# Optimization experiments

Measured on AMD Instinct MI355X. Metric: run time of the kernel, lower is better.

The kernel has to match this reference:

```python
import jax, jax.numpy as jnp
from jax import lax
import numpy as np

B, T, F, H = 1024, 512, 64, 128


def setup_inputs() -> dict:
    key = jax.random.key(0)
    ks = jax.random.split(key, 12)
    s_in = 1.0 / np.sqrt(H)  # PyTorch LSTM init scale
    inp = {
        "x": jax.random.normal(ks[0], (B, T, F), dtype=jnp.float32),
        # layer 0 (gate order i, f, g, o as in PyTorch)
        "W_ih0": jax.random.uniform(ks[1], (4 * H, F), jnp.float32, -s_in, s_in),
        "W_hh0": jax.random.uniform(ks[2], (4 * H, H), jnp.float32, -s_in, s_in),
        "b_ih0": jax.random.uniform(ks[3], (4 * H,), jnp.float32, -s_in, s_in),
        "b_hh0": jax.random.uniform(ks[4], (4 * H,), jnp.float32, -s_in, s_in),
        # layer 1
        "W_ih1": jax.random.uniform(ks[5], (4 * H, H), jnp.float32, -s_in, s_in),
        "W_hh1": jax.random.uniform(ks[6], (4 * H, H), jnp.float32, -s_in, s_in),
        "b_ih1": jax.random.uniform(ks[7], (4 * H,), jnp.float32, -s_in, s_in),
        "b_hh1": jax.random.uniform(ks[8], (4 * H,), jnp.float32, -s_in, s_in),
        # MLP head
        "fc1_w": jax.random.uniform(ks[9], (64, H), jnp.float32, -s_in, s_in),
        "fc1_b": jnp.zeros((64,), jnp.float32),
        "fc2_w": jax.random.uniform(ks[10], (1, 64), jnp.float32, -1 / 8.0, 1 / 8.0),
        "fc2_b": jnp.zeros((1,), jnp.float32),
    }
    return inp


def _lstm_layer(x_seq, W_ih, W_hh, b_ih, b_hh):
    """x_seq: [B, T, Fin] -> hidden sequence [B, T, H]. PyTorch gate order i,f,g,o."""
    Bn = x_seq.shape[0]
    Hn = W_hh.shape[1]
    # precompute input projection for all timesteps (one big GEMM)
    x_proj = jnp.einsum("btf,gf->btg", x_seq, W_ih) + b_ih + b_hh  # [B, T, 4H]

    def step(carry, xt):
        h, c = carry
        gates = xt + h @ W_hh.T  # [B, 4H]
        i, f, g, o = jnp.split(gates, 4, axis=-1)
        i = jax.nn.sigmoid(i)
        f = jax.nn.sigmoid(f)
        g = jnp.tanh(g)
        o = jax.nn.sigmoid(o)
        c = f * c + i * g
        h = o * jnp.tanh(c)
        return (h, c), h

    h0 = jnp.zeros((Bn, Hn), x_seq.dtype)
    c0 = jnp.zeros((Bn, Hn), x_seq.dtype)
    (_, _), hs = lax.scan(step, (h0, c0), jnp.swapaxes(x_proj, 0, 1))  # hs: [T, B, H]
    return jnp.swapaxes(hs, 0, 1)


def reference(x, W_ih0, W_hh0, b_ih0, b_hh0, W_ih1, W_hh1, b_ih1, b_hh1,
              fc1_w, fc1_b, fc2_w, fc2_b):
    h1 = _lstm_layer(x, W_ih0, W_hh0, b_ih0, b_hh0)   # [B, T, H]
    h2 = _lstm_layer(h1, W_ih1, W_hh1, b_ih1, b_hh1)  # [B, T, H]
    last = h2[:, -1, :]                                # [B, H]
    out = jax.nn.relu(last @ fc1_w.T + fc1_b)          # [B, 64]
    out = out @ fc2_w.T + fc2_b                        # [B, 1]
    return out
```

## Files before the change

kernel.cpp:

```cpp
#include <hip/hip_runtime.h>
#include <math.h>


#define BB 1024
#define TT 512
#define FF 64
#define HH 128
#define LOG2E 1.44269504088896340736f
#define TWOLOG2E 2.88539008177792681472f

typedef __attribute__((ext_vector_type(8))) short     v8s;
typedef __attribute__((ext_vector_type(8))) _Float16  v8h;
typedef __attribute__((ext_vector_type(4))) float     v4f;

__device__ __forceinline__ short bf16r(float v) {
    unsigned u = __float_as_uint(v);
    return (short)((u + 0x7FFFu + ((u >> 16) & 1u)) >> 16);
}
__device__ __forceinline__ float bf16tof(short s) {
    return __uint_as_float(((unsigned)(unsigned short)s) << 16);
}
__device__ __forceinline__ float rcp1p(float y) {
    return __builtin_amdgcn_rcpf(1.0f + __builtin_exp2f(y));
}
__device__ __forceinline__ void light_barrier() {
    asm volatile("s_waitcnt lgkmcnt(0)\n\ts_barrier" ::: "memory");
}
__device__ __forceinline__ void wait_flag_ge(int* f, int need) {
    for (int i = 0; i < 2000000; ++i) {
        int v = __hip_atomic_fetch_add(f, 0, __ATOMIC_ACQUIRE,
                                       __HIP_MEMORY_SCOPE_AGENT);
        if (v >= need) return;
        __builtin_amdgcn_s_sleep(4);
    }
}
__device__ __forceinline__ void split2(float a, float b,
                                       unsigned& hi, unsigned& lo) {
    unsigned ua = __float_as_uint(a), ub = __float_as_uint(b);
    hi = (ua >> 16) | (ub & 0xFFFF0000u);
    float ra = a - __uint_as_float(ua & 0xFFFF0000u);
    float rb = b - __uint_as_float(ub & 0xFFFF0000u);
    lo = (__float_as_uint(ra) >> 16) | (__float_as_uint(rb) & 0xFFFF0000u);
}


#define PROD_STEP(CUR, NXT, RD, WR, tv, PUB)                                   \
  {                                                                            \
    float2 xnew = *(const float2*)xp;                                          \
    if ((tv) < TT - 4) xp += FF;                                               \
    if ((tv) > 0) {                                                            \
      uint2 hv = *(const uint2*)&hbuf[CUR][hrow * 136 + hcol];                 \
      *(uint2*)hcs = hv;                                                       \
      hcs += (long)BB * HH;                                                    \
    }                                                                          \
    v8h ah[4];                                                                 \
    _Pragma("unroll") for (int q = 0; q < 4; ++q)                              \
        ah[q] = *(const v8h*)&hbuf[CUR][lane16 * 136 + q * 32 + quad * 8];     \
    v4f g0 = xacc[0], g1 = xacc[1], g2 = xacc[2], g3 = xacc[3];                \
    _Pragma("unroll") for (int q = 0; q < 4; ++q) {                            \
      g0 = __builtin_amdgcn_mfma_f32_16x16x32_f16(ah[q], bh[0][q], g0, 0, 0, 0);\
      g1 = __builtin_amdgcn_mfma_f32_16x16x32_f16(ah[q], bh[1][q], g1, 0, 0, 0);\
      g2 = __builtin_amdgcn_mfma_f32_16x16x32_f16(ah[q], bh[2][q], g2, 0, 0, 0);\
      g3 = __builtin_amdgcn_mfma_f32_16x16x32_f16(ah[q], bh[3][q], g3, 0, 0, 0);\
    }                                                                          \
    _Pragma("unroll") for (int r = 0; r < 4; ++r) {                            \
      float ig = rcp1p(-g0[r]);                                                \
      float fg = rcp1p(-g1[r]);                                                \
      float gt = fmaf(-2.0f, rcp1p(g2[r]), 1.0f);                              \
      float og = rcp1p(-g3[r]);                                                \
      c[r] = fmaf(fg, c[r], ig * gt);                                          \
      float th = fmaf(-2.0f, rcp1p(TWOLOG2E * c[r]), 1.0f);                    \
      float h = og * th;                                                       \
      hbuf[NXT][(quad * 4 + r) * 136 + jh] = (_Float16)h;                      \
    }                                                                          \
    {                                                                          \
      v8s xh[2], xl[2];                                                        \
      _Pragma("unroll") for (int q = 0; q < 2; ++q) {                          \
        xh[q] = *(const v8s*)&pool[RD][0][lane16 * 72 + q * 32 + quad * 8];    \
        xl[q] = *(const v8s*)&pool[RD][1][lane16 * 72 + q * 32 + quad * 8];    \
      }                                                                        \
      _Pragma("unroll") for (int g = 0; g < 4; ++g) {                          \
        v4f a = {bias[g], bias[g], bias[g], bias[g]};                          \
        a = __builtin_amdgcn_mfma_f32_16x16x32_bf16(xh[0], bxh[g][0], a, 0, 0, 0);\
        a = __builtin_amdgcn_mfma_f32_16x16x32_bf16(xh[0], bxl[g][0], a, 0, 0, 0);\
        a = __builtin_amdgcn_mfma_f32_16x16x32_bf16(xl[0], bxh[g][0], a, 0, 0, 0);\
        a = __builtin_amdgcn_mfma_f32_16x16x32_bf16(xh[1], bxh[g][1], a, 0, 0, 0);\
        a = __builtin_amdgcn_mfma_f32_16x16x32_bf16(xh[1], bxl[g][1], a, 0, 0, 0);\
        a = __builtin_amdgcn_mfma_f32_16x16x32_bf16(xl[1], bxh[g][1], a, 0, 0, 0);\
        xacc[g] = a;                                                           \
      }                                                                        \
    }                                                                          \
    {                                                                          \
      unsigned hi_, lo_;                                                       \
      split2(xreg.x, xreg.y, hi_, lo_);                                        \
      *(unsigned*)&pool[WR][0][xr_row * 72 + xr_col] = hi_;                    \
      *(unsigned*)&pool[WR][1][xr_row * 72 + xr_col] = lo_;                    \
    }                                                                          \
    xreg = xnew;                                                               \
    if (PUB) {                                                                 \
      __syncthreads();                                                         \
      if (tid == 0)                                                            \
        __hip_atomic_store(flagp, (tv), __ATOMIC_RELEASE,                      \
                           __HIP_MEMORY_SCOPE_AGENT);                          \
    } else {                                                                   \
      light_barrier();                                                         \
    }                                                                          \
  }

#define CONS_STEP(CUR, NXT, RD, WR, tv, DOWAIT)                                \
  {                                                                            \
    if (DOWAIT) {                                                              \
      if (tid == 0) wait_flag_ge(flagp, ((tv) + 15 < TT) ? (tv) + 15 : TT);    \
      light_barrier();                                                         \
    }                                                                          \
    v8h a2[4];                                                                 \
    _Pragma("unroll") for (int q = 0; q < 4; ++q)                              \
        a2[q] = *(const v8h*)&hbuf[CUR][lane16 * 136 + q * 32 + quad * 8];     \
    v4f g0 = a1acc[0], g1 = a1acc[1], g2 = a1acc[2], g3 = a1acc[3];            \
    _Pragma("unroll") for (int q = 0; q < 4; ++q) {                            \
      g0 = __builtin_amdgcn_mfma_f32_16x16x32_f16(a2[q], bh[0][q], g0, 0, 0, 0);\
      g1 = __builtin_amdgcn_mfma_f32_16x16x32_f16(a2[q], bh[1][q], g1, 0, 0, 0);\
      g2 = __builtin_amdgcn_mfma_f32_16x16x32_f16(a2[q], bh[2][q], g2, 0, 0, 0);\
      g3 = __builtin_amdgcn_mfma_f32_16x16x32_f16(a2[q], bh[3][q], g3, 0, 0, 0);\
    }                                                                          \
    _Pragma("unroll") for (int r = 0; r < 4; ++r) {                            \
      float ig = rcp1p(-g0[r]);                                                \
      float fg = rcp1p(-g1[r]);                                                \
      float gt = fmaf(-2.0f, rcp1p(g2[r]), 1.0f);                              \
      float og = rcp1p(-g3[r]);                                                \
      c[r] = fmaf(fg, c[r], ig * gt);                                          \
      float th = fmaf(-2.0f, rcp1p(TWOLOG2E * c[r]), 1.0f);                    \
      float h = og * th;                                                       \
      hbuf[NXT][(quad * 4 + r) * 136 + jh] = (_Float16)h;                      \
      if ((tv) == TT - 1) hs[(b0 + quad * 4 + r) * HH + jh] = h;               \
    }                                                                          \
    {                                                                          \
      v8h a1[4];                                                               \
      _Pragma("unroll") for (int q = 0; q < 4; ++q)                            \
          a1[q] = *(const v8h*)&sb[(RD) * 2176 + lane16 * 136 + q * 32 + quad * 8];\
      _Pragma("unroll") for (int g = 0; g < 4; ++g) {                          \
        v4f a = {bias[g], bias[g], bias[g], bias[g]};                          \
        _Pragma("unroll") for (int q = 0; q < 4; ++q)                          \
            a = __builtin_amdgcn_mfma_f32_16x16x32_f16(a1[q], bi[g][q], a, 0, 0, 0);\
        a1acc[g] = a;                                                          \
      }                                                                        \
    }                                                                          \
    *(uint2*)&sb[(WR) * 2176 + hr_row * 136 + hr_col] = hreg;                  \
    hreg = *(const uint2*)hp;                                                  \
    if ((tv) < TT - 4) hp += (long)BB * HH;                                    \
    light_barrier();                                                           \
  }

__global__ __launch_bounds__(512, 1) void fused_lstm_kernel(
    const float* __restrict__ x,
    const float* __restrict__ Wih0, const float* __restrict__ Whh0,
    const float* __restrict__ bih0, const float* __restrict__ bhh0,
    const float* __restrict__ Wih1, const float* __restrict__ Whh1,
    const float* __restrict__ bih1, const float* __restrict__ bhh1,
    _Float16* __restrict__ h1c, float* __restrict__ hs, int* __restrict__ flags)
{
    const int tid = threadIdx.x;
    const int w = tid >> 6;
    const int l = tid & 63;
    const int lane16 = l & 15;
    const int quad = l >> 4;
    const int jh = 16 * w + lane16;
    const int hrow = tid >> 5;
    const int hcol = (tid & 31) * 4;

    __shared__ __align__(16) _Float16 hbuf[2][16 * 136];
    __shared__ __align__(16) short    pool[2][2][16 * 72];

    if (blockIdx.x < 64) {
        const int tile = blockIdx.x;
        const long b0 = (long)tile * 16;
        int* flagp = &flags[tile];

        v8h bh[4][4];
        v8s bxh[4][2], bxl[4][2];
        float bias[4];
        float c[4] = {0.f, 0.f, 0.f, 0.f};

#pragma unroll
        for (int g = 0; g < 4; ++g) {
            const int col = g * 128 + jh;
            const float sg = (g == 2) ? TWOLOG2E : LOG2E;
            bias[g] = (bih0[col] + bhh0[col]) * sg;
#pragma unroll
            for (int q = 0; q < 4; ++q) {
                const float* p = &Whh0[(long)col * HH + q * 32 + quad * 8];
                float4 u0 = *(const float4*)p;
                float4 u1 = *(const float4*)(p + 4);
                v8h t;
                t[0]=(_Float16)(u0.x*sg); t[1]=(_Float16)(u0.y*sg);
                t[2]=(_Float16)(u0.z*sg); t[3]=(_Float16)(u0.w*sg);
                t[4]=(_Float16)(u1.x*sg); t[5]=(_Float16)(u1.y*sg);
                t[6]=(_Float16)(u1.z*sg); t[7]=(_Float16)(u1.w*sg);
                bh[g][q] = t;
            }
#pragma unroll
            for (int q = 0; q < 2; ++q) {
                const float* p = &Wih0[(long)col * FF + q * 32 + quad * 8];
                float4 u0 = *(const float4*)p;
                float4 u1 = *(const float4*)(p + 4);
                float vv[8] = {u0.x,u0.y,u0.z,u0.w,u1.x,u1.y,u1.z,u1.w};
                v8s hi, lo;
#pragma unroll
                for (int e = 0; e < 8; ++e) {
                    float vs = vv[e] * sg;
                    short hbits = bf16r(vs);
                    hi[e] = hbits;
                    lo[e] = bf16r(vs - bf16tof(hbits));
                }
                bxh[g][q] = hi; bxl[g][q] = lo;
            }
        }

        for (int i = tid; i < 16 * 136; i += 512) hbuf[0][i] = (_Float16)0.0f;

        const int xr_row = tid >> 5;
        const int xr_col = (tid & 31) * 2;
        const float* xp = &x[(b0 + xr_row) * TT * FF + xr_col];
        float2 x0v  = *(const float2*)xp;
        float2 x1v  = *(const float2*)(xp + FF);
        float2 xreg = *(const float2*)(xp + 2 * FF);
        xp += 3 * FF;
        {
            unsigned hi, lo; split2(x0v.x, x0v.y, hi, lo);
            *(unsigned*)&pool[0][0][xr_row * 72 + xr_col] = hi;
            *(unsigned*)&pool[0][1][xr_row * 72 + xr_col] = lo;
        }
        __syncthreads();

        v4f xacc[4];
        {
            v8s xh[2], xl[2];
#pragma unroll
            for (int q = 0; q < 2; ++q) {
                xh[q] = *(const v8s*)&pool[0][0][lane16 * 72 + q * 32 + quad * 8];
                xl[q] = *(const v8s*)&pool[0][1][lane16 * 72 + q * 32 + quad * 8];
            }
#pragma unroll
            for (int g = 0; g < 4; ++g) {
                v4f a = {bias[g], bias[g], bias[g], bias[g]};
                a = __builtin_amdgcn_mfma_f32_16x16x32_bf16(xh[0], bxh[g][0], a, 0, 0, 0);
                a = __builtin_amdgcn_mfma_f32_16x16x32_bf16(xh[0], bxl[g][0], a, 0, 0, 0);
                a = __builtin_amdgcn_mfma_f32_16x16x32_bf16(xl[0], bxh[g][0], a, 0, 0, 0);
                a = __builtin_amdgcn_mfma_f32_16x16x32_bf16(xh[1], bxh[g][1], a, 0, 0, 0);
                a = __builtin_amdgcn_mfma_f32_16x16x32_bf16(xh[1], bxl[g][1], a, 0, 0, 0);
                a = __builtin_amdgcn_mfma_f32_16x16x32_bf16(xl[1], bxh[g][1], a, 0, 0, 0);
                xacc[g] = a;
            }
        }
        {
            unsigned hi, lo; split2(x1v.x, x1v.y, hi, lo);
            *(unsigned*)&pool[1][0][xr_row * 72 + xr_col] = hi;
            *(unsigned*)&pool[1][1][xr_row * 72 + xr_col] = lo;
        }
        light_barrier();

        _Float16* hcs = h1c + (b0 + hrow) * HH + hcol;

        for (int tp = 0; tp < TT / 2; ++tp) {
            PROD_STEP(0, 1, 1, 0, 2 * tp,     false);
            PROD_STEP(1, 0, 0, 1, 2 * tp + 1, ((tp & 3) == 3));
        }
        {
            uint2 hv = *(const uint2*)&hbuf[0][hrow * 136 + hcol];
            *(uint2*)hcs = hv;
        }
        __syncthreads();
        if (tid == 0)
            __hip_atomic_store(flagp, TT, __ATOMIC_RELEASE,
                               __HIP_MEMORY_SCOPE_AGENT);
    } else {
        const int tile = blockIdx.x - 64;
        const long b0 = (long)tile * 16;
        int* flagp = &flags[tile];

        v8h bi[4][4], bh[4][4];
        float bias[4];
        float c[4] = {0.f, 0.f, 0.f, 0.f};

#pragma unroll
        for (int g = 0; g < 4; ++g) {
            const int col = g * 128 + jh;
            const float sg = (g == 2) ? TWOLOG2E : LOG2E;
            bias[g] = (bih1[col] + bhh1[col]) * sg;
#pragma unroll
            for (int q = 0; q < 4; ++q) {
                const float* pi = &Wih1[(long)col * HH + q * 32 + quad * 8];
                float4 u0 = *(const float4*)pi;
                float4 u1 = *(const float4*)(pi + 4);
                v8h t;
                t[0]=(_Float16)(u0.x*sg); t[1]=(_Float16)(u0.y*sg);
                t[2]=(_Float16)(u0.z*sg); t[3]=(_Float16)(u0.w*sg);
                t[4]=(_Float16)(u1.x*sg); t[5]=(_Float16)(u1.y*sg);
                t[6]=(_Float16)(u1.z*sg); t[7]=(_Float16)(u1.w*sg);
                bi[g][q] = t;
                const float* ph = &Whh1[(long)col * HH + q * 32 + quad * 8];
                float4 v0 = *(const float4*)ph;
                float4 v1 = *(const float4*)(ph + 4);
                v8h s;
                s[0]=(_Float16)(v0.x*sg); s[1]=(_Float16)(v0.y*sg);
                s[2]=(_Float16)(v0.z*sg); s[3]=(_Float16)(v0.w*sg);
                s[4]=(_Float16)(v1.x*sg); s[5]=(_Float16)(v1.y*sg);
                s[6]=(_Float16)(v1.z*sg); s[7]=(_Float16)(v1.w*sg);
                bh[g][q] = s;
            }
        }

        for (int i = tid; i < 16 * 136; i += 512) hbuf[0][i] = (_Float16)0.0f;

        _Float16* sb = (_Float16*)&pool[0][0][0];

        const int hr_row = tid >> 5;
        const int hr_col = (tid & 31) * 4;

        if (tid == 0) wait_flag_ge(flagp, 15);
        __syncthreads();

        const _Float16* hp = h1c + (b0 + hr_row) * HH + hr_col;
        uint2 h0v  = *(const uint2*)hp;
        uint2 h1v  = *(const uint2*)(hp + (long)BB * HH);
        uint2 hreg = *(const uint2*)(hp + 2L * BB * HH);
        hp += 3L * BB * HH;
        *(uint2*)&sb[0 * 2176 + hr_row * 136 + hr_col] = h0v;
        __syncthreads();

        v4f a1acc[4];
        {
            v8h a1[4];
#pragma unroll
            for (int q = 0; q < 4; ++q)
                a1[q] = *(const v8h*)&sb[0 * 2176 + lane16 * 136 + q * 32 + quad * 8];
#pragma unroll
            for (int g = 0; g < 4; ++g) {
                v4f a = {bias[g], bias[g], bias[g], bias[g]};
#pragma unroll
                for (int q = 0; q < 4; ++q)
                    a = __builtin_amdgcn_mfma_f32_16x16x32_f16(a1[q], bi[g][q], a, 0, 0, 0);
                a1acc[g] = a;
            }
        }
        *(uint2*)&sb[1 * 2176 + hr_row * 136 + hr_col] = h1v;
        light_barrier();

        for (int tp = 0; tp < TT / 2; ++tp) {
            CONS_STEP(0, 1, 1, 0, 2 * tp,     ((tp & 3) == 0 && tp > 0));
            CONS_STEP(1, 0, 0, 1, 2 * tp + 1, false);
        }
    }
}

__global__ __launch_bounds__(64) void head_kernel(
    const float* __restrict__ h, const float* __restrict__ w1,
    const float* __restrict__ b1, const float* __restrict__ w2,
    const float* __restrict__ b2, float* __restrict__ out)
{
    const int b = blockIdx.x;
    const int n = threadIdx.x;
    float acc = b1[n];
#pragma unroll
    for (int k = 0; k < HH; ++k)
        acc = fmaf(w1[n * HH + k], h[b * HH + k], acc);
    float v = fmaxf(acc, 0.0f) * w2[n];
#pragma unroll
    for (int off = 32; off > 0; off >>= 1)
        v += __shfl_down(v, off);
    if (n == 0) out[b] = v + b2[0];
}

extern "C" void kernel_launch(void* const* d_in, const int* in_sizes, int n_in,
                              void* d_out, int out_size, void* d_ws, size_t ws_size,
                              hipStream_t stream)
{
    const float* x    = (const float*)d_in[0];
    const float* Wih0 = (const float*)d_in[1];
    const float* Whh0 = (const float*)d_in[2];
    const float* bih0 = (const float*)d_in[3];
    const float* bhh0 = (const float*)d_in[4];
    const float* Wih1 = (const float*)d_in[5];
    const float* Whh1 = (const float*)d_in[6];
    const float* bih1 = (const float*)d_in[7];
    const float* bhh1 = (const float*)d_in[8];
    const float* w1   = (const float*)d_in[9];
    const float* b1   = (const float*)d_in[10];
    const float* w2   = (const float*)d_in[11];
    const float* b2   = (const float*)d_in[12];
    float* out = (float*)d_out;

    char* ws = (char*)d_ws;
    _Float16* h1c = (_Float16*)ws;
    float* hs  = (float*)(ws + (size_t)BB * TT * HH * sizeof(_Float16));
    int* flags = (int*)(ws + (size_t)BB * TT * HH * sizeof(_Float16)
                           + (size_t)BB * HH * sizeof(float));

    hipMemsetAsync(flags, 0, 64 * sizeof(int), stream);

    fused_lstm_kernel<<<128, 512, 0, stream>>>(
        x, Wih0, Whh0, bih0, bhh0, Wih1, Whh1, bih1, bhh1, h1c, hs, flags);
    head_kernel<<<BB, 64, 0, stream>>>(hs, w1, b1, w2, b2, out);
}
```

Baseline: 886.5 us.

## Split each block into recurrent and helper warp groups for input projection

Each block grows to 1024 threads. Half the threads run the serial recurrence: h@W_hh, the gate math, and the c/h update. The other half compute the next step's input projection (x@W_ih or h1@W_ih1) into a shared xbuf, and also handle the global loads and stores. The goal is to take the input-projection MFMAs and memory traffic off the recurrence's critical path. The cost is more shared memory, barriers that now span 16 waves, and helper and recurrent groups that must stay in lockstep through matching barrier counts, which is fragile.

```diff
diff --git a/kernel.cpp b/kernel.cpp
--- a/kernel.cpp
+++ b/kernel.cpp
@@ -25,6 +25,9 @@
 }
 __device__ __forceinline__ void light_barrier() {
     asm volatile("s_waitcnt lgkmcnt(0)\n\ts_barrier" ::: "memory");
+}
+__device__ __forceinline__ void heavy_barrier() {
+    asm volatile("s_waitcnt vmcnt(0) lgkmcnt(0)\n\ts_barrier" ::: "memory");
 }
 __device__ __forceinline__ void wait_flag_ge(int* f, int need) {
     for (int i = 0; i < 2000000; ++i) {
@@ -44,19 +47,15 @@
 }
 
 
-#define PROD_STEP(CUR, NXT, RD, WR, tv, PUB)                                   \
+#define REC_STEP(CUR, NXT, tv, STORE_HS)                                       \
   {                                                                            \
-    float2 xnew = *(const float2*)xp;                                          \
-    if ((tv) < TT - 4) xp += FF;                                               \
-    if ((tv) > 0) {                                                            \
-      uint2 hv = *(const uint2*)&hbuf[CUR][hrow * 136 + hcol];                 \
-      *(uint2*)hcs = hv;                                                       \
-      hcs += (long)BB * HH;                                                    \
-    }                                                                          \
+    v4f g0 = *(const v4f*)&xbuf[CUR][(0 * 128 + jh) * 20 + quad * 4];          \
+    v4f g1 = *(const v4f*)&xbuf[CUR][(1 * 128 + jh) * 20 + quad * 4];          \
+    v4f g2 = *(const v4f*)&xbuf[CUR][(2 * 128 + jh) * 20 + quad * 4];          \
+    v4f g3 = *(const v4f*)&xbuf[CUR][(3 * 128 + jh) * 20 + quad * 4];          \
     v8h ah[4];                                                                 \
     _Pragma("unroll") for (int q = 0; q < 4; ++q)                              \
         ah[q] = *(const v8h*)&hbuf[CUR][lane16 * 136 + q * 32 + quad * 8];     \
-    v4f g0 = xacc[0], g1 = xacc[1], g2 = xacc[2], g3 = xacc[3];                \
     _Pragma("unroll") for (int q = 0; q < 4; ++q) {                            \
       g0 = __builtin_amdgcn_mfma_f32_16x16x32_f16(ah[q], bh[0][q], g0, 0, 0, 0);\
       g1 = __builtin_amdgcn_mfma_f32_16x16x32_f16(ah[q], bh[1][q], g1, 0, 0, 0);\
@@ -72,86 +71,61 @@
       float th = fmaf(-2.0f, rcp1p(TWOLOG2E * c[r]), 1.0f);                    \
       float h = og * th;                                                       \
       hbuf[NXT][(quad * 4 + r) * 136 + jh] = (_Float16)h;                      \
-    }                                                                          \
-    {                                                                          \
-      v8s xh[2], xl[2];                                                        \
-      _Pragma("unroll") for (int q = 0; q < 2; ++q) {                          \
-        xh[q] = *(const v8s*)&pool[RD][0][lane16 * 72 + q * 32 + quad * 8];    \
-        xl[q] = *(const v8s*)&pool[RD][1][lane16 * 72 + q * 32 + quad * 8];    \
-      }                                                                        \
-      _Pragma("unroll") for (int g = 0; g < 4; ++g) {                          \
-        v4f a = {bias[g], bias[g], bias[g], bias[g]};                          \
-        a = __builtin_amdgcn_mfma_f32_16x16x32_bf16(xh[0], bxh[g][0], a, 0, 0, 0);\
-        a = __builtin_amdgcn_mfma_f32_16x16x32_bf16(xh[0], bxl[g][0], a, 0, 0, 0);\
-        a = __builtin_amdgcn_mfma_f32_16x16x32_bf16(xl[0], bxh[g][0], a, 0, 0, 0);\
-        a = __builtin_amdgcn_mfma_f32_16x16x32_bf16(xh[1], bxh[g][1], a, 0, 0, 0);\
-        a = __builtin_amdgcn_mfma_f32_16x16x32_bf16(xh[1], bxl[g][1], a, 0, 0, 0);\
-        a = __builtin_amdgcn_mfma_f32_16x16x32_bf16(xl[1], bxh[g][1], a, 0, 0, 0);\
-        xacc[g] = a;                                                           \
-      }                                                                        \
+      if ((STORE_HS) && (tv) == TT - 1)                                        \
+        hs[(b0 + quad * 4 + r) * HH + jh] = h;                                 \
+    }                                                                          \
+  }
+
+#define PHELP_STEP(CUR, NXT, tv)                                               \
+  {                                                                            \
+    float2 xnew = *(const float2*)xp;                                          \
+    if ((tv) < TT - 4) xp += FF;                                               \
+    if ((tv) > 0) {                                                            \
+      uint2 hv = *(const uint2*)&hbuf[CUR][hr_row * 136 + hr_col];             \
+      *(uint2*)hcs = hv;                                                       \
+      hcs += (long)BB * HH;                                                    \
+    }                                                                          \
+    v8s xh[2], xl[2];                                                          \
+    _Pragma("unroll") for (int q = 0; q < 2; ++q) {                            \
+      xh[q] = *(const v8s*)&pool[NXT][0][lane16 * 72 + q * 32 + quad * 8];     \
+      xl[q] = *(const v8s*)&pool[NXT][1][lane16 * 72 + q * 32 + quad * 8];     \
+    }                                                                          \
+    _Pragma("unroll") for (int g = 0; g < 4; ++g) {                            \
+      v4f a = {bias[g], bias[g], bias[g], bias[g]};                            \
+      a = __builtin_amdgcn_mfma_f32_16x16x32_bf16(xh[0], bxh[g][0], a, 0, 0, 0);\
+      a = __builtin_amdgcn_mfma_f32_16x16x32_bf16(xh[0], bxl[g][0], a, 0, 0, 0);\
+      a = __builtin_amdgcn_mfma_f32_16x16x32_bf16(xl[0], bxh[g][0], a, 0, 0, 0);\
+      a = __builtin_amdgcn_mfma_f32_16x16x32_bf16(xh[1], bxh[g][1], a, 0, 0, 0);\
+      a = __builtin_amdgcn_mfma_f32_16x16x32_bf16(xh[1], bxl[g][1], a, 0, 0, 0);\
+      a = __builtin_amdgcn_mfma_f32_16x16x32_bf16(xl[1], bxh[g][1], a, 0, 0, 0);\
+      *(v4f*)&xbuf[NXT][(g * 128 + jh) * 20 + quad * 4] = a;                   \
     }                                                                          \
     {                                                                          \
       unsigned hi_, lo_;                                                       \
       split2(xreg.x, xreg.y, hi_, lo_);                                        \
-      *(unsigned*)&pool[WR][0][xr_row * 72 + xr_col] = hi_;                    \
-      *(unsigned*)&pool[WR][1][xr_row * 72 + xr_col] = lo_;                    \
+      *(unsigned*)&pool[CUR][0][xr_row * 72 + xr_col] = hi_;                   \
+      *(unsigned*)&pool[CUR][1][xr_row * 72 + xr_col] = lo_;                   \
     }                                                                          \
     xreg = xnew;                                                               \
-    if (PUB) {                                                                 \
-      __syncthreads();                                                         \
-      if (tid == 0)                                                            \
-        __hip_atomic_store(flagp, (tv), __ATOMIC_RELEASE,                      \
-                           __HIP_MEMORY_SCOPE_AGENT);                          \
-    } else {                                                                   \
-      light_barrier();                                                         \
-    }                                                                          \
   }
 
-#define CONS_STEP(CUR, NXT, RD, WR, tv, DOWAIT)                                \
+#define CHELP_STEP(CUR, NXT, tv)                                               \
   {                                                                            \
-    if (DOWAIT) {                                                              \
-      if (tid == 0) wait_flag_ge(flagp, ((tv) + 15 < TT) ? (tv) + 15 : TT);    \
-      light_barrier();                                                         \
-    }                                                                          \
-    v8h a2[4];                                                                 \
+    v8h a1[4];                                                                 \
     _Pragma("unroll") for (int q = 0; q < 4; ++q)                              \
-        a2[q] = *(const v8h*)&hbuf[CUR][lane16 * 136 + q * 32 + quad * 8];     \
-    v4f g0 = a1acc[0], g1 = a1acc[1], g2 = a1acc[2], g3 = a1acc[3];            \
-    _Pragma("unroll") for (int q = 0; q < 4; ++q) {                            \
-      g0 = __builtin_amdgcn_mfma_f32_16x16x32_f16(a2[q], bh[0][q], g0, 0, 0, 0);\
-      g1 = __builtin_amdgcn_mfma_f32_16x16x32_f16(a2[q], bh[1][q], g1, 0, 0, 0);\
-      g2 = __builtin_amdgcn_mfma_f32_16x16x32_f16(a2[q], bh[2][q], g2, 0, 0, 0);\
-      g3 = __builtin_amdgcn_mfma_f32_16x16x32_f16(a2[q], bh[3][q], g3, 0, 0, 0);\
-    }                                                                          \
-    _Pragma("unroll") for (int r = 0; r < 4; ++r) {                            \
-      float ig = rcp1p(-g0[r]);                                                \
-      float fg = rcp1p(-g1[r]);                                                \
-      float gt = fmaf(-2.0f, rcp1p(g2[r]), 1.0f);                              \
-      float og = rcp1p(-g3[r]);                                                \
-      c[r] = fmaf(fg, c[r], ig * gt);                                          \
-      float th = fmaf(-2.0f, rcp1p(TWOLOG2E * c[r]), 1.0f);                    \
-      float h = og * th;                                                       \
-      hbuf[NXT][(quad * 4 + r) * 136 + jh] = (_Float16)h;                      \
-      if ((tv) == TT - 1) hs[(b0 + quad * 4 + r) * HH + jh] = h;               \
-    }                                                                          \
-    {                                                                          \
-      v8h a1[4];                                                               \
+        a1[q] = *(const v8h*)&sb[(NXT) * 2176 + lane16 * 136 + q * 32 + quad * 8];\
+    _Pragma("unroll") for (int g = 0; g < 4; ++g) {                            \
+      v4f a = {bias[g], bias[g], bias[g], bias[g]};                            \
       _Pragma("unroll") for (int q = 0; q < 4; ++q)                            \
-          a1[q] = *(const v8h*)&sb[(RD) * 2176 + lane16 * 136 + q * 32 + quad * 8];\
-      _Pragma("unroll") for (int g = 0; g < 4; ++g) {                          \
-        v4f a = {bias[g], bias[g], bias[g], bias[g]};                          \
-        _Pragma("unroll") for (int q = 0; q < 4; ++q)                          \
-            a = __builtin_amdgcn_mfma_f32_16x16x32_f16(a1[q], bi[g][q], a, 0, 0, 0);\
-        a1acc[g] = a;                                                          \
-      }                                                                        \
-    }                                                                          \
-    *(uint2*)&sb[(WR) * 2176 + hr_row * 136 + hr_col] = hreg;                  \
+          a = __builtin_amdgcn_mfma_f32_16x16x32_f16(a1[q], bi[g][q], a, 0, 0, 0);\
+      *(v4f*)&xbuf[NXT][(g * 128 + jh) * 20 + quad * 4] = a;                   \
+    }                                                                          \
+    *(uint2*)&sb[(CUR) * 2176 + hr_row * 136 + hr_col] = hreg;                 \
     hreg = *(const uint2*)hp;                                                  \
     if ((tv) < TT - 4) hp += (long)BB * HH;                                    \
-    light_barrier();                                                           \
   }
 
-__global__ __launch_bounds__(512, 1) void fused_lstm_kernel(
+__global__ __launch_bounds__(1024, 1) void fused_lstm_kernel(
     const float* __restrict__ x,
     const float* __restrict__ Wih0, const float* __restrict__ Whh0,
     const float* __restrict__ bih0, const float* __restrict__ bhh0,
@@ -160,195 +134,236 @@
     _Float16* __restrict__ h1c, float* __restrict__ hs, int* __restrict__ flags)
 {
     const int tid = threadIdx.x;
-    const int w = tid >> 6;
+    const bool isrec = tid < 512;
     const int l = tid & 63;
     const int lane16 = l & 15;
     const int quad = l >> 4;
-    const int jh = 16 * w + lane16;
-    const int hrow = tid >> 5;
-    const int hcol = (tid & 31) * 4;
+    const int jh = 16 * ((tid >> 6) & 7) + lane16;
+    const int stid = tid & 511;
+    const int hr_row = stid >> 5;
+    const int hr_col = (stid & 31) * 4;
 
     __shared__ __align__(16) _Float16 hbuf[2][16 * 136];
     __shared__ __align__(16) short    pool[2][2][16 * 72];
+    __shared__ __align__(16) float    xbuf[2][512 * 20];
 
     if (blockIdx.x < 64) {
         const int tile = blockIdx.x;
         const long b0 = (long)tile * 16;
         int* flagp = &flags[tile];
 
-        v8h bh[4][4];
-        v8s bxh[4][2], bxl[4][2];
-        float bias[4];
-        float c[4] = {0.f, 0.f, 0.f, 0.f};
-
-#pragma unroll
-        for (int g = 0; g < 4; ++g) {
-            const int col = g * 128 + jh;
-            const float sg = (g == 2) ? TWOLOG2E : LOG2E;
-            bias[g] = (bih0[col] + bhh0[col]) * sg;
-#pragma unroll
-            for (int q = 0; q < 4; ++q) {
-                const float* p = &Whh0[(long)col * HH + q * 32 + quad * 8];
-                float4 u0 = *(const float4*)p;
-                float4 u1 = *(const float4*)(p + 4);
-                v8h t;
-                t[0]=(_Float16)(u0.x*sg); t[1]=(_Float16)(u0.y*sg);
-                t[2]=(_Float16)(u0.z*sg); t[3]=(_Float16)(u0.w*sg);
-                t[4]=(_Float16)(u1.x*sg); t[5]=(_Float16)(u1.y*sg);
-                t[6]=(_Float16)(u1.z*sg); t[7]=(_Float16)(u1.w*sg);
-                bh[g][q] = t;
-            }
-#pragma unroll
-            for (int q = 0; q < 2; ++q) {
-                const float* p = &Wih0[(long)col * FF + q * 32 + quad * 8];
-                float4 u0 = *(const float4*)p;
-                float4 u1 = *(const float4*)(p + 4);
-                float vv[8] = {u0.x,u0.y,u0.z,u0.w,u1.x,u1.y,u1.z,u1.w};
-                v8s hi, lo;
-#pragma unroll
-                for (int e = 0; e < 8; ++e) {
-                    float vs = vv[e] * sg;
-                    short hbits = bf16r(vs);
-                    hi[e] = hbits;
-                    lo[e] = bf16r(vs - bf16tof(hbits));
-                }
-                bxh[g][q] = hi; bxl[g][q] = lo;
-            }
+        if (isrec) {
+            v8h bh[4][4];
+#pragma unroll
+            for (int g = 0; g < 4; ++g) {
+                const int col = g * 128 + jh;
+                const float sg = (g == 2) ? TWOLOG2E : LOG2E;
+#pragma unroll
+                for (int q = 0; q < 4; ++q) {
+                    const float* p = &Whh0[(long)col * HH + q * 32 + quad * 8];
+                    float4 u0 = *(const float4*)p;
+                    float4 u1 = *(const float4*)(p + 4);
+                    v8h t;
+                    t[0]=(_Float16)(u0.x*sg); t[1]=(_Float16)(u0.y*sg);
+                    t[2]=(_Float16)(u0.z*sg); t[3]=(_Float16)(u0.w*sg);
+                    t[4]=(_Float16)(u1.x*sg); t[5]=(_Float16)(u1.y*sg);
+                    t[6]=(_Float16)(u1.z*sg); t[7]=(_Float16)(u1.w*sg);
+                    bh[g][q] = t;
+                }
+            }
+            for (int i = tid; i < 16 * 136; i += 512) hbuf[0][i] = (_Float16)0.0f;
+            float c[4] = {0.f, 0.f, 0.f, 0.f};
+            __syncthreads();
+            light_barrier();
+
+            for (int tp = 0; tp < TT / 2; ++tp) {
+                REC_STEP(0, 1, 2 * tp, 0);
+                light_barrier();
+                REC_STEP(1, 0, 2 * tp + 1, 0);
+                light_barrier();
+                if ((tp & 3) == 3 && tid == 0)
+                    __hip_atomic_store(flagp, 2 * tp + 1, __ATOMIC_RELEASE,
+                                       __HIP_MEMORY_SCOPE_AGENT);
+            }
+            light_barrier();
+            if (tid == 0)
+                __hip_atomic_store(flagp, TT, __ATOMIC_RELEASE,
+                                   __HIP_MEMORY_SCOPE_AGENT);
+        } else {
+            float bias[4];
+            v8s bxh[4][2], bxl[4][2];
+#pragma unroll
+            for (int g = 0; g < 4; ++g) {
+                const int col = g * 128 + jh;
+                const float sg = (g == 2) ? TWOLOG2E : LOG2E;
+                bias[g] = (bih0[col] + bhh0[col]) * sg;
+#pragma unroll
+                for (int q = 0; q < 2; ++q) {
+                    const float* p = &Wih0[(long)col * FF + q * 32 + quad * 8];
+                    float4 u0 = *(const float4*)p;
+                    float4 u1 = *(const float4*)(p + 4);
+                    float vv[8] = {u0.x,u0.y,u0.z,u0.w,u1.x,u1.y,u1.z,u1.w};
+                    v8s hi, lo;
+#pragma unroll
+                    for (int e = 0; e < 8; ++e) {
+                        float vs = vv[e] * sg;
+                        short hbits = bf16r(vs);
+                        hi[e] = hbits;
+                        lo[e] = bf16r(vs - bf16tof(hbits));
+                    }
+                    bxh[g][q] = hi; bxl[g][q] = lo;
+                }
+            }
+            const int xr_row = stid >> 5;
+            const int xr_col = (stid & 31) * 2;
+            const float* xp = &x[(b0 + xr_row) * TT * FF + xr_col];
+            float2 x0v  = *(const float2*)xp;
+            float2 x1v  = *(const float2*)(xp + FF);
+            float2 xreg = *(const float2*)(xp + 2 * FF);
+            xp += 3 * FF;
+            {
+                unsigned hi, lo; split2(x0v.x, x0v.y, hi, lo);
+                *(unsigned*)&pool[0][0][xr_row * 72 + xr_col] = hi;
+                *(unsigned*)&pool[0][1][xr_row * 72 + xr_col] = lo;
+            }
+            __syncthreads();
+            {
+                v8s xh[2], xl[2];
+#pragma unroll
+                for (int q = 0; q < 2; ++q) {
+                    xh[q] = *(const v8s*)&pool[0][0][lane16 * 72 + q * 32 + quad * 8];
+                    xl[q] = *(const v8s*)&pool[0][1][lane16 * 72 + q * 32 + quad * 8];
+                }
+#pragma unroll
+                for (int g = 0; g < 4; ++g) {
+                    v4f a = {bias[g], bias[g], bias[g], bias[g]};
+                    a = __builtin_amdgcn_mfma_f32_16x16x32_bf16(xh[0], bxh[g][0], a, 0, 0, 0);
+                    a = __builtin_amdgcn_mfma_f32_16x16x32_bf16(xh[0], bxl[g][0], a, 0, 0, 0);
+                    a = __builtin_amdgcn_mfma_f32_16x16x32_bf16(xl[0], bxh[g][0], a, 0, 0, 0);
+                    a = __builtin_amdgcn_mfma_f32_16x16x32_bf16(xh[1], bxh[g][1], a, 0, 0, 0);
+                    a = __builtin_amdgcn_mfma_f32_16x16x32_bf16(xh[1], bxl[g][1], a, 0, 0, 0);
+                    a = __builtin_amdgcn_mfma_f32_16x16x32_bf16(xl[1], bxh[g][1], a, 0, 0, 0);
+                    *(v4f*)&xbuf[0][(g * 128 + jh) * 20 + quad * 4] = a;
+                }
+            }
+            {
+                unsigned hi, lo; split2(x1v.x, x1v.y, hi, lo);
+                *(unsigned*)&pool[1][0][xr_row * 72 + xr_col] = hi;
+                *(unsigned*)&pool[1][1][xr_row * 72 + xr_col] = lo;
+            }
+            light_barrier();
+
+            _Float16* hcs = h1c + (b0 + hr_row) * HH + hr_col;
+            for (int tp = 0; tp < TT / 2; ++tp) {
+                PHELP_STEP(0, 1, 2 * tp);
+                light_barrier();
+                PHELP_STEP(1, 0, 2 * tp + 1);
+                if ((tp & 3) == 3) heavy_barrier();
+                else               light_barrier();
+            }
+            {
+                uint2 hv = *(const uint2*)&hbuf[0][hr_row * 136 + hr_col];
+                *(uint2*)hcs = hv;
+            }
+            heavy_barrier();
         }
-
-        for (int i = tid; i < 16 * 136; i += 512) hbuf[0][i] = (_Float16)0.0f;
-
-        const int xr_row = tid >> 5;
-        const int xr_col = (tid & 31) * 2;
-        const float* xp = &x[(b0 + xr_row) * TT * FF + xr_col];
-        float2 x0v  = *(const float2*)xp;
-        float2 x1v  = *(const float2*)(xp + FF);
-        float2 xreg = *(const float2*)(xp + 2 * FF);
-        xp += 3 * FF;
-        {
-            unsigned hi, lo; split2(x0v.x, x0v.y, hi, lo);
-            *(unsigned*)&pool[0][0][xr_row * 72 + xr_col] = hi;
-            *(unsigned*)&pool[0][1][xr_row * 72 + xr_col] = lo;
-        }
-        __syncthreads();
-
-        v4f xacc[4];
-        {
-            v8s xh[2], xl[2];
-#pragma unroll
-            for (int q = 0; q < 2; ++q) {
-                xh[q] = *(const v8s*)&pool[0][0][lane16 * 72 + q * 32 + quad * 8];
-                xl[q] = *(const v8s*)&pool[0][1][lane16 * 72 + q * 32 + quad * 8];
-            }
-#pragma unroll
-            for (int g = 0; g < 4; ++g) {
-                v4f a = {bias[g], bias[g], bias[g], bias[g]};
-                a = __builtin_amdgcn_mfma_f32_16x16x32_bf16(xh[0], bxh[g][0], a, 0, 0, 0);
-                a = __builtin_amdgcn_mfma_f32_16x16x32_bf16(xh[0], bxl[g][0], a, 0, 0, 0);
-                a = __builtin_amdgcn_mfma_f32_16x16x32_bf16(xl[0], bxh[g][0], a, 0, 0, 0);
-                a = __builtin_amdgcn_mfma_f32_16x16x32_bf16(xh[1], bxh[g][1], a, 0, 0, 0);
-                a = __builtin_amdgcn_mfma_f32_16x16x32_bf16(xh[1], bxl[g][1], a, 0, 0, 0);
-                a = __builtin_amdgcn_mfma_f32_16x16x32_bf16(xl[1], bxh[g][1], a, 0, 0, 0);
-                xacc[g] = a;
-            }
-        }
-        {
-            unsigned hi, lo; split2(x1v.x, x1v.y, hi, lo);
-            *(unsigned*)&pool[1][0][xr_row * 72 + xr_col] = hi;
-            *(unsigned*)&pool[1][1][xr_row * 72 + xr_col] = lo;
-        }
-        light_barrier();
-
-        _Float16* hcs = h1c + (b0 + hrow) * HH + hcol;
-
-        for (int tp = 0; tp < TT / 2; ++tp) {
-            PROD_STEP(0, 1, 1, 0, 2 * tp,     false);
-            PROD_STEP(1, 0, 0, 1, 2 * tp + 1, ((tp & 3) == 3));
-        }
-        {
-            uint2 hv = *(const uint2*)&hbuf[0][hrow * 136 + hcol];
-            *(uint2*)hcs = hv;
-        }
-        __syncthreads();
-        if (tid == 0)
-            __hip_atomic_store(flagp, TT, __ATOMIC_RELEASE,
-                               __HIP_MEMORY_SCOPE_AGENT);
     } else {
         const int tile = blockIdx.x - 64;
         const long b0 = (long)tile * 16;
         int* flagp = &flags[tile];
-
-        v8h bi[4][4], bh[4][4];
-        float bias[4];
-        float c[4] = {0.f, 0.f, 0.f, 0.f};
-
-#pragma unroll
-        for (int g = 0; g < 4; ++g) {
-            const int col = g * 128 + jh;
-            const float sg = (g == 2) ? TWOLOG2E : LOG2E;
-            bias[g] = (bih1[col] + bhh1[col]) * sg;
-#pragma unroll
-            for (int q = 0; q < 4; ++q) {
-                const float* pi = &Wih1[(long)col * HH + q * 32 + quad * 8];
-                float4 u0 = *(const float4*)pi;
-                float4 u1 = *(const float4*)(pi + 4);
-                v8h t;
-                t[0]=(_Float16)(u0.x*sg); t[1]=(_Float16)(u0.y*sg);
-                t[2]=(_Float16)(u0.z*sg); t[3]=(_Float16)(u0.w*sg);
-                t[4]=(_Float16)(u1.x*sg); t[5]=(_Float16)(u1.y*sg);
-                t[6]=(_Float16)(u1.z*sg); t[7]=(_Float16)(u1.w*sg);
-                bi[g][q] = t;
-                const float* ph = &Whh1[(long)col * HH + q * 32 + quad * 8];
-                float4 v0 = *(const float4*)ph;
-                float4 v1 = *(const float4*)(ph + 4);
-                v8h s;
-                s[0]=(_Float16)(v0.x*sg); s[1]=(_Float16)(v0.y*sg);
-                s[2]=(_Float16)(v0.z*sg); s[3]=(_Float16)(v0.w*sg);
-                s[4]=(_Float16)(v1.x*sg); s[5]=(_Float16)(v1.y*sg);
-                s[6]=(_Float16)(v1.z*sg); s[7]=(_Float16)(v1.w*sg);
-                bh[g][q] = s;
-            }
-        }
-
-        for (int i = tid; i < 16 * 136; i += 512) hbuf[0][i] = (_Float16)0.0f;
-
         _Float16* sb = (_Float16*)&pool[0][0][0];
 
-        const int hr_row = tid >> 5;
-        const int hr_col = (tid & 31) * 4;
-
-        if (tid == 0) wait_flag_ge(flagp, 15);
-        __syncthreads();
-
-        const _Float16* hp = h1c + (b0 + hr_row) * HH + hr_col;
-        uint2 h0v  = *(const uint2*)hp;
-        uint2 h1v  = *(const uint2*)(hp + (long)BB * HH);
-        uint2 hreg = *(const uint2*)(hp + 2L * BB * HH);
-        hp += 3L * BB * HH;
-        *(uint2*)&sb[0 * 2176 + hr_row * 136 + hr_col] = h0v;
-        __syncthreads();
-
-        v4f a1acc[4];
-        {
-            v8h a1[4];
-#pragma unroll
-            for (int q = 0; q < 4; ++q)
-                a1[q] = *(const v8h*)&sb[0 * 2176 + lane16 * 136 + q * 32 + quad * 8];
+        if (isrec) {
+            v8h bh[4][4];
 #pragma unroll
             for (int g = 0; g < 4; ++g) {
-                v4f a = {bias[g], bias[g], bias[g], bias[g]};
+                const int col = g * 128 + jh;
+                const float sg = (g == 2) ? TWOLOG2E : LOG2E;
+#pragma unroll
+                for (int q = 0; q < 4; ++q) {
+                    const float* ph = &Whh1[(long)col * HH + q * 32 + quad * 8];
+                    float4 v0 = *(const float4*)ph;
+                    float4 v1 = *(const float4*)(ph + 4);
+                    v8h s;
+                    s[0]=(_Float16)(v0.x*sg); s[1]=(_Float16)(v0.y*sg);
+                    s[2]=(_Float16)(v0.z*sg); s[3]=(_Float16)(v0.w*sg);
+                    s[4]=(_Float16)(v1.x*sg); s[5]=(_Float16)(v1.y*sg);
+                    s[6]=(_Float16)(v1.z*sg); s[7]=(_Float16)(v1.w*sg);
+                    bh[g][q] = s;
+                }
+            }
+            for (int i = tid; i < 16 * 136; i += 512) hbuf[0][i] = (_Float16)0.0f;
+            float c[4] = {0.f, 0.f, 0.f, 0.f};
+            if (tid == 0) wait_flag_ge(flagp, 15);
+            __syncthreads();
+            light_barrier();
+            light_barrier();
+
+            for (int tp = 0; tp < TT / 2; ++tp) {
+                if ((tp & 3) == 0 && tp > 0) {
+                    if (tid == 0)
+                        wait_flag_ge(flagp, (2 * tp + 15 < TT) ? 2 * tp + 15 : TT);
+                    light_barrier();
+                }
+                REC_STEP(0, 1, 2 * tp, 1);
+                light_barrier();
+                REC_STEP(1, 0, 2 * tp + 1, 1);
+                light_barrier();
+            }
+        } else {
+            float bias[4];
+            v8h bi[4][4];
+#pragma unroll
+            for (int g = 0; g < 4; ++g) {
+                const int col = g * 128 + jh;
+                const float sg = (g == 2) ? TWOLOG2E : LOG2E;
+                bias[g] = (bih1[col] + bhh1[col]) * sg;
+#pragma unroll
+                for (int q = 0; q < 4; ++q) {
+                    const float* pi = &Wih1[(long)col * HH + q * 32 + quad * 8];
+                    float4 u0 = *(const float4*)pi;
+                    float4 u1 = *(const float4*)(pi + 4);
+                    v8h t;
+                    t[0]=(_Float16)(u0.x*sg); t[1]=(_Float16)(u0.y*sg);
+                    t[2]=(_Float16)(u0.z*sg); t[3]=(_Float16)(u0.w*sg);
+                    t[4]=(_Float16)(u1.x*sg); t[5]=(_Float16)(u1.y*sg);
+                    t[6]=(_Float16)(u1.z*sg); t[7]=(_Float16)(u1.w*sg);
+                    bi[g][q] = t;
+                }
+            }
+            __syncthreads();
+
+            const _Float16* hp = h1c + (b0 + hr_row) * HH + hr_col;
+            uint2 h0v  = *(const uint2*)hp;
+            uint2 h1v  = *(const uint2*)(hp + (long)BB * HH);
+            uint2 hreg = *(const uint2*)(hp + 2L * BB * HH);
+            hp += 3L * BB * HH;
+            *(uint2*)&sb[0 * 2176 + hr_row * 136 + hr_col] = h0v;
+            light_barrier();
+            {
+                v8h a1[4];
 #pragma unroll
                 for (int q = 0; q < 4; ++q)
-                    a = __builtin_amdgcn_mfma_f32_16x16x32_f16(a1[q], bi[g][q], a, 0, 0, 0);
-                a1acc[g] = a;
-            }
-        }
-        *(uint2*)&sb[1 * 2176 + hr_row * 136 + hr_col] = h1v;
-        light_barrier();
-
-        for (int tp = 0; tp < TT / 2; ++tp) {
-            CONS_STEP(0, 1, 1, 0, 2 * tp,     ((tp & 3) == 0 && tp > 0));
-            CONS_STEP(1, 0, 0, 1, 2 * tp + 1, false);
+                    a1[q] = *(const v8h*)&sb[0 * 2176 + lane16 * 136 + q * 32 + quad * 8];
+#pragma unroll
+                for (int g = 0; g < 4; ++g) {
+                    v4f a = {bias[g], bias[g], bias[g], bias[g]};
+#pragma unroll
+                    for (int q = 0; q < 4; ++q)
+                        a = __builtin_amdgcn_mfma_f32_16x16x32_f16(a1[q], bi[g][q], a, 0, 0, 0);
+                    *(v4f*)&xbuf[0][(g * 128 + jh) * 20 + quad * 4] = a;
+                }
+            }
+            *(uint2*)&sb[1 * 2176 + hr_row * 136 + hr_col] = h1v;
+            light_barrier();
+
+            for (int tp = 0; tp < TT / 2; ++tp) {
+                if ((tp & 3) == 0 && tp > 0) light_barrier();
+                CHELP_STEP(0, 1, 2 * tp);
+                light_barrier();
+                CHELP_STEP(1, 0, 2 * tp + 1);
+                light_barrier();
+            }
         }
     }
 }
@@ -398,7 +413,7 @@
 
     hipMemsetAsync(flags, 0, 64 * sizeof(int), stream);
 
-    fused_lstm_kernel<<<128, 512, 0, stream>>>(
+    fused_lstm_kernel<<<128, 1024, 0, stream>>>(
         x, Wih0, Whh0, bih0, bhh0, Wih1, Whh1, bih1, bhh1, h1c, hs, flags);
     head_kernel<<<BB, 64, 0, stream>>>(hs, w1, b1, w2, b2, out);
 }
```

After: 873.6 us. About the same (-1.4%).
